# Optimization experiments

Measured on AMD Instinct MI355X. Metric: run time of the kernel, lower is better.

The kernel has to match this reference:

```python
import jax, jax.numpy as jnp
import numpy as np

# Fixed by JastrowNet source: ElectronicSchNet(n_interactions=2, kernel_dim=8, embedding_dim=16, version=1)
BATCH = 512
N_UP, N_DOWN = 16, 16
N_ELEC = N_UP + N_DOWN
N_ATOMS = 8
DIST_FEAT = 32
KERNEL = 8
EMBED = 16
N_LAYERS = 2
W_HIDDEN = 16  # log-spaced hidden dim of the w filter MLP: round(sqrt(32*8))
N_CHAN = 3     # same-spin, anti-spin, nuclear filter channels


def ssp(x):
    # shifted softplus used by SchNet
    return jax.nn.softplus(x) - jnp.log(2.0).astype(x.dtype)


def setup_inputs() -> dict:
    key = jax.random.key(0)
    ks = jax.random.split(key, 16)
    s = lambda fan_in: 1.0 / np.sqrt(fan_in)
    inp = {
        # Gaussian-expanded distance features are non-negative
        'edges_elec': jax.random.uniform(ks[0], (BATCH, N_ELEC, N_ELEC, DIST_FEAT), jnp.float32),
        'edges_nuc': jax.random.uniform(ks[1], (BATCH, N_ELEC, N_ATOMS, DIST_FEAT), jnp.float32),
        # electron spin embedding table (up=0, down=1) and nuclear embeddings Y
        'X_emb': jax.random.normal(ks[2], (2, EMBED), jnp.float32),
        'Y': jax.random.normal(ks[3], (N_ATOMS, KERNEL), jnp.float32),
        # per-layer, per-channel w filter MLP (dist_feat -> hidden -> kernel)
        'wW1': jax.random.normal(ks[4], (N_LAYERS, N_CHAN, DIST_FEAT, W_HIDDEN), jnp.float32) * s(DIST_FEAT),
        'wb1': jnp.zeros((N_LAYERS, N_CHAN, W_HIDDEN), jnp.float32),
        'wW2': jax.random.normal(ks[5], (N_LAYERS, N_CHAN, W_HIDDEN, KERNEL), jnp.float32) * s(W_HIDDEN),
        'wb2': jnp.zeros((N_LAYERS, N_CHAN, KERNEL), jnp.float32),
        # per-layer h subnet (embed -> kernel) and g subnet (kernel -> embed)
        'hW': jax.random.normal(ks[6], (N_LAYERS, EMBED, KERNEL), jnp.float32) * s(EMBED),
        'hb': jnp.zeros((N_LAYERS, KERNEL), jnp.float32),
        'gW': jax.random.normal(ks[7], (N_LAYERS, KERNEL, EMBED), jnp.float32) * s(KERNEL),
        'gb': jnp.zeros((N_LAYERS, EMBED), jnp.float32),
        # readout: Linear(16, 1, bias=False)
        'orb_W': jax.random.normal(ks[8], (EMBED,), jnp.float32) * s(EMBED),
    }
    return inp


def reference(edges_elec, edges_nuc, X_emb, Y, wW1, wb1, wW2, wb2, hW, hb, gW, gb, orb_W):
    B = edges_elec.shape[0]
    spins = jnp.concatenate([jnp.zeros(N_UP, jnp.int32), jnp.ones(N_DOWN, jnp.int32)])
    not_self = ~jnp.eye(N_ELEC, dtype=bool)
    same = ((spins[:, None] == spins[None, :]) & not_self)  # [n,n]
    anti = (spins[:, None] != spins[None, :])

    # initial electron embeddings by spin, broadcast over batch
    x = jnp.broadcast_to(X_emb[spins], (B, N_ELEC, EMBED))

    for l in range(N_LAYERS):
        def w_sub(e, c):
            h1 = ssp(e @ wW1[l, c] + wb1[l, c])
            return ssp(h1 @ wW2[l, c] + wb2[l, c])  # [..., KERNEL]

        w_same = w_sub(edges_elec, 0) * same[None, :, :, None]  # [B,n,n,k]
        w_anti = w_sub(edges_elec, 1) * anti[None, :, :, None]
        w_n = w_sub(edges_nuc, 2)                                # [B,n,m,k]

        hx = ssp(x @ hW[l] + hb[l])                              # [B,n,k]
        # continuous-filter message passing: gather neighbor features, multiply by filter, scatter-sum
        z = jnp.einsum('bijk,bjk->bik', w_same + w_anti, hx)
        z = z + jnp.einsum('bimk,mk->bik', w_n, Y)
        # version 1: single g applied to combined message, residual update
        x = x + z @ gW[l] + gb[l]

    # orbital readout Linear(16,1,bias=False).squeeze(-1).sum(-1)
    return (x @ orb_W).sum(axis=-1)  # [B]
```

## Files before the change

### kernel.cpp

```cpp
#include <hip/hip_runtime.h>
#include <hip/hip_bf16.h>
#include <cstddef>


#define NB   512
#define NE   32
#define NA   8
#define NF   32
#define NH   16
#define NK   8
#define NEMB 16

__device__ __forceinline__ float ssp(float v){
    return fmaxf(v, 0.f) + __logf(1.f + __expf(-fabsf(v))) - 0.6931471805599453f;
}

__device__ __forceinline__ void compute_w(const float4 ev[8],
        const float* __restrict__ sW1, const float* __restrict__ sB1,
        const float* __restrict__ sW2, const float* __restrict__ sB2,
        float w[NK])
{
    float h1[NH];
#pragma unroll
    for (int h = 0; h < NH; h++) h1[h] = sB1[h];
#pragma unroll
    for (int q = 0; q < 8; q++){
        float e4[4] = {ev[q].x, ev[q].y, ev[q].z, ev[q].w};
#pragma unroll
        for (int c = 0; c < 4; c++){
            const float ef = e4[c];
            const float4* w4 = (const float4*)(sW1 + (4*q + c)*NH);
#pragma unroll
            for (int t = 0; t < 4; t++){
                float4 wv = w4[t];
                h1[4*t+0] = fmaf(ef, wv.x, h1[4*t+0]);
                h1[4*t+1] = fmaf(ef, wv.y, h1[4*t+1]);
                h1[4*t+2] = fmaf(ef, wv.z, h1[4*t+2]);
                h1[4*t+3] = fmaf(ef, wv.w, h1[4*t+3]);
            }
        }
    }
#pragma unroll
    for (int h = 0; h < NH; h++) h1[h] = ssp(h1[h]);
    float acc[NK];
#pragma unroll
    for (int k = 0; k < NK; k++) acc[k] = sB2[k];
#pragma unroll
    for (int h = 0; h < NH; h++){
        const float hv = h1[h];
        const float4* w4 = (const float4*)(sW2 + h*NK);
#pragma unroll
        for (int t = 0; t < 2; t++){
            float4 wv = w4[t];
            acc[4*t+0] = fmaf(hv, wv.x, acc[4*t+0]);
            acc[4*t+1] = fmaf(hv, wv.y, acc[4*t+1]);
            acc[4*t+2] = fmaf(hv, wv.z, acc[4*t+2]);
            acc[4*t+3] = fmaf(hv, wv.w, acc[4*t+3]);
        }
    }
#pragma unroll
    for (int k = 0; k < NK; k++) w[k] = ssp(acc[k]);
}

extern "C" __global__ void __launch_bounds__(256, 4)
filters_kernel(const float* __restrict__ edges_elec,
               const float* __restrict__ edges_nuc,
               const float* __restrict__ X_emb,
               const float* __restrict__ Yk,
               const float* __restrict__ wW1, const float* __restrict__ wb1,
               const float* __restrict__ wW2, const float* __restrict__ wb2,
               const float* __restrict__ hW,  const float* __restrict__ hb,
               __hip_bfloat16* __restrict__ w2out,
               float* __restrict__ z1p,
               float* __restrict__ zn1, float* __restrict__ zn2)
{
    __shared__ __align__(16) float s_W1[2*NF*NH];
    __shared__ __align__(16) float s_b1[2*NH];
    __shared__ __align__(16) float s_W2[2*NH*NK];
    __shared__ __align__(16) float s_b2[2*NK];
    __shared__ float s_hx1[2*NK];
    __shared__ float s_Y[NA*NK];

    const int bid = blockIdx.x, t = threadIdx.x;
    const int p = bid >> 9, b = bid & 511;
    const bool isNuc = (p == 4);
    const int qi = p >> 1, qj = p & 1;
    const int cc = isNuc ? 2 : ((qi == qj) ? 0 : 1);

    for (int idx = t; idx < 2*NF*NH; idx += 256){
        int l = idx >> 9, r = idx & 511;
        s_W1[idx] = wW1[(l*3 + cc)*NF*NH + r];
    }
    if (t < 2*NH*NK){
        int l = t >> 7, r = t & 127;
        s_W2[t] = wW2[(l*3 + cc)*NH*NK + r];
    }
    if (t < 2*NH){ int l = t >> 4, r = t & 15; s_b1[t] = wb1[(l*3 + cc)*NH + r]; }
    if (t < 2*NK){ int l = t >> 3, r = t & 7;  s_b2[t] = wb2[(l*3 + cc)*NK + r]; }
    if (isNuc){
        if (t < NA*NK) s_Y[t] = Yk[t];
    } else if (t < 2*NK){
        int s = t >> 3, k = t & 7;
        float acc = hb[k];
#pragma unroll
        for (int e = 0; e < NEMB; e++)
            acc = fmaf(X_emb[s*NEMB + e], hW[e*NK + k], acc);
        s_hx1[t] = ssp(acc);
    }
    __syncthreads();

    const float* src;
    if (isNuc) src = edges_nuc + ((size_t)b*NE*NA + t) * NF;
    else {
        int i = qi*16 + (t >> 4), j = qj*16 + (t & 15);
        src = edges_elec + ((size_t)b*NE*NE + i*NE + j) * NF;
    }
    float4 ev[8];
    {
        const float4* p4 = (const float4*)src;
#pragma unroll
        for (int q = 0; q < 8; q++) ev[q] = p4[q];
    }

    {
        float w[NK];
        compute_w(ev, s_W1, s_b1, s_W2, s_b2, w);
        if (isNuc){
            const int m = t & 7, i = t >> 3;
            float pk[NK];
#pragma unroll
            for (int k = 0; k < NK; k++) pk[k] = w[k] * s_Y[m*NK + k];
#pragma unroll
            for (int off = 4; off > 0; off >>= 1)
#pragma unroll
                for (int k = 0; k < NK; k++) pk[k] += __shfl_down(pk[k], off, 8);
            if (m == 0){
#pragma unroll
                for (int k = 0; k < NK; k++) zn1[((size_t)b*NE + i)*NK + k] = pk[k];
            }
        } else {
            const int i16 = t >> 4, j16 = t & 15;
            const float msk = (cc == 0 && i16 == j16) ? 0.f : 1.f;
            float pk[NK];
#pragma unroll
            for (int k = 0; k < NK; k++) pk[k] = w[k] * msk * s_hx1[qj*NK + k];
#pragma unroll
            for (int off = 8; off > 0; off >>= 1)
#pragma unroll
                for (int k = 0; k < NK; k++) pk[k] += __shfl_down(pk[k], off, 16);
            if (j16 == 0){
                const int i = qi*16 + i16;
#pragma unroll
                for (int k = 0; k < NK; k++)
                    z1p[(((size_t)b*2 + qj)*NE + i)*NK + k] = pk[k];
            }
        }
    }
    {
        float w[NK];
        compute_w(ev, s_W1 + NF*NH, s_b1 + NH, s_W2 + NH*NK, s_b2 + NK, w);
        if (isNuc){
            const int m = t & 7, i = t >> 3;
            float pk[NK];
#pragma unroll
            for (int k = 0; k < NK; k++) pk[k] = w[k] * s_Y[m*NK + k];
#pragma unroll
            for (int off = 4; off > 0; off >>= 1)
#pragma unroll
                for (int k = 0; k < NK; k++) pk[k] += __shfl_down(pk[k], off, 8);
            if (m == 0){
#pragma unroll
                for (int k = 0; k < NK; k++) zn2[((size_t)b*NE + i)*NK + k] = pk[k];
            }
        } else {
            const int i16 = t >> 4, j16 = t & 15;
            const float msk = (cc == 0 && i16 == j16) ? 0.f : 1.f;
            const int i = qi*16 + i16, j = qj*16 + j16;
            union { __hip_bfloat16 h[8]; uint4 u; } pack;
#pragma unroll
            for (int k = 0; k < NK; k++) pack.h[k] = __float2bfloat16(w[k] * msk);
            *(uint4*)&w2out[((size_t)b*NE*NE + i*NE + j)*NK] = pack.u;
        }
    }
}

extern "C" __global__ void __launch_bounds__(256, 4)
update_kernel(const float* __restrict__ X_emb,
              const float* __restrict__ hW,  const float* __restrict__ hb,
              const float* __restrict__ gW,  const float* __restrict__ gb,
              const float* __restrict__ orbW,
              const __hip_bfloat16* __restrict__ w2,
              const float* __restrict__ z1p,
              const float* __restrict__ zn1, const float* __restrict__ zn2,
              float* __restrict__ out)
{
    __shared__ float s_x[NE*NEMB];
    __shared__ float s_z[NE*NK];
    __shared__ float s_hx[NE*NK];
    __shared__ float s_gW[2*NK*NEMB];
    __shared__ float s_gb[2*NEMB];
    __shared__ float s_hW1[NEMB*NK];
    __shared__ float s_hb1[NK];
    __shared__ float s_orb[NEMB];
    __shared__ float s_red[4];

    const int b = blockIdx.x, t = threadIdx.x;

    s_gW[t] = gW[t];
    if (t < 2*NEMB)  s_gb[t]  = gb[t];
    if (t < NEMB*NK) s_hW1[t] = hW[NEMB*NK + t];
    if (t < NK)      s_hb1[t] = hb[NK + t];
    if (t < NEMB)    s_orb[t] = orbW[t];
    {
        const int i = t >> 3, k = t & 7;
        s_z[t] = z1p[(((size_t)b*2 + 0)*NE + i)*NK + k]
               + z1p[(((size_t)b*2 + 1)*NE + i)*NK + k]
               + zn1[((size_t)b*NE + i)*NK + k];
    }
    __syncthreads();
#pragma unroll
    for (int q = 0; q < 2; q++){
        const int idx = q*256 + t, i = idx >> 4, e = idx & 15;
        float acc = s_gb[e];
#pragma unroll
        for (int k = 0; k < NK; k++)
            acc = fmaf(s_z[i*NK + k], s_gW[k*NEMB + e], acc);
        s_x[idx] = X_emb[(i >> 4)*NEMB + e] + acc;
    }
    __syncthreads();
    {
        const int i = t >> 3, k = t & 7;
        float acc = s_hb1[k];
#pragma unroll
        for (int e = 0; e < NEMB; e++)
            acc = fmaf(s_x[i*NEMB + e], s_hW1[e*NK + k], acc);
        s_hx[t] = ssp(acc);
    }
    __syncthreads();
    {
        const int i16 = t >> 4, j16 = t & 15;
#pragma unroll
        for (int qh = 0; qh < 2; qh++){
            const int i = qh*16 + i16;
            float zacc[NK];
#pragma unroll
            for (int k = 0; k < NK; k++) zacc[k] = 0.f;
#pragma unroll
            for (int qj = 0; qj < 2; qj++){
                const int j = qj*16 + j16;
                union { uint4 u; __hip_bfloat16 h[8]; } raw;
                raw.u = *(const uint4*)&w2[((size_t)b*NE*NE + i*NE + j)*NK];
                float pk[NK];
#pragma unroll
                for (int k = 0; k < NK; k++)
                    pk[k] = __bfloat162float(raw.h[k]) * s_hx[j*NK + k];
#pragma unroll
                for (int off = 8; off > 0; off >>= 1)
#pragma unroll
                    for (int k = 0; k < NK; k++) pk[k] += __shfl_down(pk[k], off, 16);
#pragma unroll
                for (int k = 0; k < NK; k++) zacc[k] += pk[k];
            }
            if (j16 == 0){
#pragma unroll
                for (int k = 0; k < NK; k++) s_z[i*NK + k] = zacc[k];
            }
        }
    }
    __syncthreads();
    { const int i = t >> 3, k = t & 7; s_z[t] += zn2[((size_t)b*NE + i)*NK + k]; }
    __syncthreads();
#pragma unroll
    for (int q = 0; q < 2; q++){
        const int idx = q*256 + t, i = idx >> 4, e = idx & 15;
        float acc = s_gb[NEMB + e];
#pragma unroll
        for (int k = 0; k < NK; k++)
            acc = fmaf(s_z[i*NK + k], s_gW[NK*NEMB + k*NEMB + e], acc);
        s_x[idx] += acc;
    }
    __syncthreads();
    float part = (s_x[t] + s_x[t + 256]) * s_orb[t & 15];
#pragma unroll
    for (int off = 32; off > 0; off >>= 1) part += __shfl_down(part, off, 64);
    if ((t & 63) == 0) s_red[t >> 6] = part;
    __syncthreads();
    if (t == 0) out[b] = s_red[0] + s_red[1] + s_red[2] + s_red[3];
}

extern "C" void kernel_launch(void* const* d_in, const int* in_sizes, int n_in,
                              void* d_out, int out_size, void* d_ws, size_t ws_size,
                              hipStream_t stream)
{
    const float* edges_elec = (const float*)d_in[0];
    const float* edges_nuc  = (const float*)d_in[1];
    const float* X_emb      = (const float*)d_in[2];
    const float* Yk         = (const float*)d_in[3];
    const float* wW1        = (const float*)d_in[4];
    const float* wb1        = (const float*)d_in[5];
    const float* wW2        = (const float*)d_in[6];
    const float* wb2        = (const float*)d_in[7];
    const float* hW         = (const float*)d_in[8];
    const float* hb         = (const float*)d_in[9];
    const float* gW         = (const float*)d_in[10];
    const float* gb         = (const float*)d_in[11];
    const float* orbW       = (const float*)d_in[12];

    char* ws = (char*)d_ws;
    __hip_bfloat16* w2 = (__hip_bfloat16*)ws;
    float* z1p = (float*)(ws + 8388608);
    float* zn1 = (float*)(ws + 8388608 + 1048576);
    float* zn2 = (float*)(ws + 8388608 + 1048576 + 524288);

    filters_kernel<<<5*NB, 256, 0, stream>>>(
        edges_elec, edges_nuc, X_emb, Yk, wW1, wb1, wW2, wb2, hW, hb,
        w2, z1p, zn1, zn2);
    update_kernel<<<NB, 256, 0, stream>>>(
        X_emb, hW, hb, gW, gb, orbW, w2, z1p, zn1, zn2, (float*)d_out);
}
```

Before: 157.8 us.

## Fuse filter and update kernels via per-batch atomic last-block completion

Merges the two launches into one kernel. Each of the five blocks per batch element increments a global counter, and the last block to finish runs the update and readout stage for that batch. Filter weights are now read straight from global memory (scalar loads) instead of being staged in LDS, and the layer-2 message sum is done per-thread over j instead of with shuffle reductions. This removes one launch and the inter-kernel gap, at the cost of a serial tail in the last block and relying on threadfence/atomic ordering.

```diff
diff --git a/kernel.cpp b/kernel.cpp
--- a/kernel.cpp
+++ b/kernel.cpp
@@ -11,75 +11,73 @@
 #define NK   8
 #define NEMB 16
 
+#define Z1P_OFF  8388608u
+#define ZN1_OFF  (Z1P_OFF + 1048576u)
+#define ZN2_OFF  (ZN1_OFF + 524288u)
+
+__device__ int g_cnt[NB];
+
 __device__ __forceinline__ float ssp(float v){
     return fmaxf(v, 0.f) + __logf(1.f + __expf(-fabsf(v))) - 0.6931471805599453f;
 }
 
 __device__ __forceinline__ void compute_w(const float4 ev[8],
-        const float* __restrict__ sW1, const float* __restrict__ sB1,
-        const float* __restrict__ sW2, const float* __restrict__ sB2,
+        const float* __restrict__ W1, const float* __restrict__ B1,
+        const float* __restrict__ W2, const float* __restrict__ B2,
         float w[NK])
 {
     float h1[NH];
 #pragma unroll
-    for (int h = 0; h < NH; h++) h1[h] = sB1[h];
+    for (int h = 0; h < NH; h++) h1[h] = B1[h];
 #pragma unroll
     for (int q = 0; q < 8; q++){
-        float e4[4] = {ev[q].x, ev[q].y, ev[q].z, ev[q].w};
+        const float e4[4] = {ev[q].x, ev[q].y, ev[q].z, ev[q].w};
 #pragma unroll
         for (int c = 0; c < 4; c++){
             const float ef = e4[c];
-            const float4* w4 = (const float4*)(sW1 + (4*q + c)*NH);
-#pragma unroll
-            for (int t = 0; t < 4; t++){
-                float4 wv = w4[t];
-                h1[4*t+0] = fmaf(ef, wv.x, h1[4*t+0]);
-                h1[4*t+1] = fmaf(ef, wv.y, h1[4*t+1]);
-                h1[4*t+2] = fmaf(ef, wv.z, h1[4*t+2]);
-                h1[4*t+3] = fmaf(ef, wv.w, h1[4*t+3]);
-            }
+            const float* wr = W1 + (4*q + c)*NH;
+#pragma unroll
+            for (int h = 0; h < NH; h++) h1[h] = fmaf(ef, wr[h], h1[h]);
         }
     }
 #pragma unroll
     for (int h = 0; h < NH; h++) h1[h] = ssp(h1[h]);
     float acc[NK];
 #pragma unroll
-    for (int k = 0; k < NK; k++) acc[k] = sB2[k];
+    for (int k = 0; k < NK; k++) acc[k] = B2[k];
 #pragma unroll
     for (int h = 0; h < NH; h++){
         const float hv = h1[h];
-        const float4* w4 = (const float4*)(sW2 + h*NK);
-#pragma unroll
-        for (int t = 0; t < 2; t++){
-            float4 wv = w4[t];
-            acc[4*t+0] = fmaf(hv, wv.x, acc[4*t+0]);
-            acc[4*t+1] = fmaf(hv, wv.y, acc[4*t+1]);
-            acc[4*t+2] = fmaf(hv, wv.z, acc[4*t+2]);
-            acc[4*t+3] = fmaf(hv, wv.w, acc[4*t+3]);
-        }
+        const float* wr = W2 + h*NK;
+#pragma unroll
+        for (int k = 0; k < NK; k++) acc[k] = fmaf(hv, wr[k], acc[k]);
     }
 #pragma unroll
     for (int k = 0; k < NK; k++) w[k] = ssp(acc[k]);
 }
 
 extern "C" __global__ void __launch_bounds__(256, 4)
-filters_kernel(const float* __restrict__ edges_elec,
-               const float* __restrict__ edges_nuc,
-               const float* __restrict__ X_emb,
-               const float* __restrict__ Yk,
-               const float* __restrict__ wW1, const float* __restrict__ wb1,
-               const float* __restrict__ wW2, const float* __restrict__ wb2,
-               const float* __restrict__ hW,  const float* __restrict__ hb,
-               __hip_bfloat16* __restrict__ w2out,
-               float* __restrict__ z1p,
-               float* __restrict__ zn1, float* __restrict__ zn2)
+jastrow_fused(const float* __restrict__ edges_elec,
+              const float* __restrict__ edges_nuc,
+              const float* __restrict__ X_emb,
+              const float* __restrict__ Yk,
+              const float* __restrict__ wW1, const float* __restrict__ wb1,
+              const float* __restrict__ wW2, const float* __restrict__ wb2,
+              const float* __restrict__ hW,  const float* __restrict__ hb,
+              const float* __restrict__ gW,  const float* __restrict__ gb,
+              const float* __restrict__ orbW,
+              __hip_bfloat16* __restrict__ w2,
+              float* __restrict__ z1p,
+              float* __restrict__ zn1, float* __restrict__ zn2,
+              float* __restrict__ out)
 {
-    __shared__ __align__(16) float s_W1[2*NF*NH];
-    __shared__ __align__(16) float s_b1[2*NH];
-    __shared__ __align__(16) float s_W2[2*NH*NK];
-    __shared__ __align__(16) float s_b2[2*NK];
-    __shared__ float s_hx1[2*NK];
+    __shared__ float s_hx1[NK];
     __shared__ float s_Y[NA*NK];
+    __shared__ float s_x[NE*NEMB];
+    __shared__ float s_z[NE*NK];
+    __shared__ float s_hx[NE*NK];
+    __shared__ float s_red[4];
+    __shared__ int   s_last;
 
     const int bid = blockIdx.x, t = threadIdx.x;
     const int p = bid >> 9, b = bid & 511;
@@ -87,24 +85,22 @@
     const int qi = p >> 1, qj = p & 1;
     const int cc = isNuc ? 2 : ((qi == qj) ? 0 : 1);
 
-    for (int idx = t; idx < 2*NF*NH; idx += 256){
-        int l = idx >> 9, r = idx & 511;
-        s_W1[idx] = wW1[(l*3 + cc)*NF*NH + r];
-    }
-    if (t < 2*NH*NK){
-        int l = t >> 7, r = t & 127;
-        s_W2[t] = wW2[(l*3 + cc)*NH*NK + r];
-    }
-    if (t < 2*NH){ int l = t >> 4, r = t & 15; s_b1[t] = wb1[(l*3 + cc)*NH + r]; }
-    if (t < 2*NK){ int l = t >> 3, r = t & 7;  s_b2[t] = wb2[(l*3 + cc)*NK + r]; }
+    const float* W1l0 = wW1 + (0*3 + cc)*NF*NH;
+    const float* W1l1 = wW1 + (1*3 + cc)*NF*NH;
+    const float* B1l0 = wb1 + (0*3 + cc)*NH;
+    const float* B1l1 = wb1 + (1*3 + cc)*NH;
+    const float* W2l0 = wW2 + (0*3 + cc)*NH*NK;
+    const float* W2l1 = wW2 + (1*3 + cc)*NH*NK;
+    const float* B2l0 = wb2 + (0*3 + cc)*NK;
+    const float* B2l1 = wb2 + (1*3 + cc)*NK;
+
     if (isNuc){
         if (t < NA*NK) s_Y[t] = Yk[t];
-    } else if (t < 2*NK){
-        int s = t >> 3, k = t & 7;
-        float acc = hb[k];
+    } else if (t < NK){
+        float acc = hb[t];
 #pragma unroll
         for (int e = 0; e < NEMB; e++)
-            acc = fmaf(X_emb[s*NEMB + e], hW[e*NK + k], acc);
+            acc = fmaf(X_emb[qj*NEMB + e], hW[e*NK + t], acc);
         s_hx1[t] = ssp(acc);
     }
     __syncthreads();
@@ -112,7 +108,7 @@
     const float* src;
     if (isNuc) src = edges_nuc + ((size_t)b*NE*NA + t) * NF;
     else {
-        int i = qi*16 + (t >> 4), j = qj*16 + (t & 15);
+        const int i = qi*16 + (t >> 4), j = qj*16 + (t & 15);
         src = edges_elec + ((size_t)b*NE*NE + i*NE + j) * NF;
     }
     float4 ev[8];
@@ -124,9 +120,9 @@
 
     {
         float w[NK];
-        compute_w(ev, s_W1, s_b1, s_W2, s_b2, w);
+        compute_w(ev, W1l0, B1l0, W2l0, B2l0, w);
         if (isNuc){
-            const int m = t & 7, i = t >> 3;
+            const int i = t >> 3, m = t & 7;
             float pk[NK];
 #pragma unroll
             for (int k = 0; k < NK; k++) pk[k] = w[k] * s_Y[m*NK + k];
@@ -143,7 +139,7 @@
             const float msk = (cc == 0 && i16 == j16) ? 0.f : 1.f;
             float pk[NK];
 #pragma unroll
-            for (int k = 0; k < NK; k++) pk[k] = w[k] * msk * s_hx1[qj*NK + k];
+            for (int k = 0; k < NK; k++) pk[k] = w[k] * msk * s_hx1[k];
 #pragma unroll
             for (int off = 8; off > 0; off >>= 1)
 #pragma unroll
@@ -158,9 +154,9 @@
     }
     {
         float w[NK];
-        compute_w(ev, s_W1 + NF*NH, s_b1 + NH, s_W2 + NH*NK, s_b2 + NK, w);
+        compute_w(ev, W1l1, B1l1, W2l1, B2l1, w);
         if (isNuc){
-            const int m = t & 7, i = t >> 3;
+            const int i = t >> 3, m = t & 7;
             float pk[NK];
 #pragma unroll
             for (int k = 0; k < NK; k++) pk[k] = w[k] * s_Y[m*NK + k];
@@ -179,108 +175,66 @@
             union { __hip_bfloat16 h[8]; uint4 u; } pack;
 #pragma unroll
             for (int k = 0; k < NK; k++) pack.h[k] = __float2bfloat16(w[k] * msk);
-            *(uint4*)&w2out[((size_t)b*NE*NE + i*NE + j)*NK] = pack.u;
+            *(uint4*)&w2[((size_t)b*NE*NE + i*NE + j)*NK] = pack.u;
         }
     }
-}
-
-extern "C" __global__ void __launch_bounds__(256, 4)
-update_kernel(const float* __restrict__ X_emb,
-              const float* __restrict__ hW,  const float* __restrict__ hb,
-              const float* __restrict__ gW,  const float* __restrict__ gb,
-              const float* __restrict__ orbW,
-              const __hip_bfloat16* __restrict__ w2,
-              const float* __restrict__ z1p,
-              const float* __restrict__ zn1, const float* __restrict__ zn2,
-              float* __restrict__ out)
-{
-    __shared__ float s_x[NE*NEMB];
-    __shared__ float s_z[NE*NK];
-    __shared__ float s_hx[NE*NK];
-    __shared__ float s_gW[2*NK*NEMB];
-    __shared__ float s_gb[2*NEMB];
-    __shared__ float s_hW1[NEMB*NK];
-    __shared__ float s_hb1[NK];
-    __shared__ float s_orb[NEMB];
-    __shared__ float s_red[4];
-
-    const int b = blockIdx.x, t = threadIdx.x;
-
-    s_gW[t] = gW[t];
-    if (t < 2*NEMB)  s_gb[t]  = gb[t];
-    if (t < NEMB*NK) s_hW1[t] = hW[NEMB*NK + t];
-    if (t < NK)      s_hb1[t] = hb[NK + t];
-    if (t < NEMB)    s_orb[t] = orbW[t];
-    {
-        const int i = t >> 3, k = t & 7;
-        s_z[t] = z1p[(((size_t)b*2 + 0)*NE + i)*NK + k]
-               + z1p[(((size_t)b*2 + 1)*NE + i)*NK + k]
-               + zn1[((size_t)b*NE + i)*NK + k];
-    }
+
+    __threadfence();
+    __syncthreads();
+    if (t == 0){
+        const int old = atomicAdd(&g_cnt[b], 1);
+        s_last = (old == 4) ? 1 : 0;
+        if (old == 4) atomicExch(&g_cnt[b], 0);
+    }
+    __syncthreads();
+    if (!s_last) return;
+    __threadfence();
+
+    s_z[t] = z1p[((size_t)b*2 + 0)*NE*NK + t]
+           + z1p[((size_t)b*2 + 1)*NE*NK + t]
+           + zn1[(size_t)b*NE*NK + t];
     __syncthreads();
 #pragma unroll
     for (int q = 0; q < 2; q++){
         const int idx = q*256 + t, i = idx >> 4, e = idx & 15;
-        float acc = s_gb[e];
+        float acc = gb[e];
 #pragma unroll
         for (int k = 0; k < NK; k++)
-            acc = fmaf(s_z[i*NK + k], s_gW[k*NEMB + e], acc);
+            acc = fmaf(s_z[i*NK + k], gW[k*NEMB + e], acc);
         s_x[idx] = X_emb[(i >> 4)*NEMB + e] + acc;
     }
     __syncthreads();
     {
         const int i = t >> 3, k = t & 7;
-        float acc = s_hb1[k];
+        float acc = hb[NK + k];
 #pragma unroll
         for (int e = 0; e < NEMB; e++)
-            acc = fmaf(s_x[i*NEMB + e], s_hW1[e*NK + k], acc);
+            acc = fmaf(s_x[i*NEMB + e], hW[NEMB*NK + e*NK + k], acc);
         s_hx[t] = ssp(acc);
     }
     __syncthreads();
     {
-        const int i16 = t >> 4, j16 = t & 15;
-#pragma unroll
-        for (int qh = 0; qh < 2; qh++){
-            const int i = qh*16 + i16;
-            float zacc[NK];
-#pragma unroll
-            for (int k = 0; k < NK; k++) zacc[k] = 0.f;
-#pragma unroll
-            for (int qj = 0; qj < 2; qj++){
-                const int j = qj*16 + j16;
-                union { uint4 u; __hip_bfloat16 h[8]; } raw;
-                raw.u = *(const uint4*)&w2[((size_t)b*NE*NE + i*NE + j)*NK];
-                float pk[NK];
-#pragma unroll
-                for (int k = 0; k < NK; k++)
-                    pk[k] = __bfloat162float(raw.h[k]) * s_hx[j*NK + k];
-#pragma unroll
-                for (int off = 8; off > 0; off >>= 1)
-#pragma unroll
-                    for (int k = 0; k < NK; k++) pk[k] += __shfl_down(pk[k], off, 16);
-#pragma unroll
-                for (int k = 0; k < NK; k++) zacc[k] += pk[k];
-            }
-            if (j16 == 0){
-#pragma unroll
-                for (int k = 0; k < NK; k++) s_z[i*NK + k] = zacc[k];
-            }
-        }
-    }
-    __syncthreads();
-    { const int i = t >> 3, k = t & 7; s_z[t] += zn2[((size_t)b*NE + i)*NK + k]; }
+        const int i = t >> 3, k = t & 7;
+        const __hip_bfloat16* wrow = w2 + ((size_t)b*NE*NE + i*NE)*NK + k;
+        float acc = zn2[(size_t)b*NE*NK + t];
+#pragma unroll
+        for (int j = 0; j < NE; j++)
+            acc = fmaf(__bfloat162float(wrow[j*NK]), s_hx[j*NK + k], acc);
+        __syncthreads();
+        s_z[t] = acc;
+    }
     __syncthreads();
 #pragma unroll
     for (int q = 0; q < 2; q++){
         const int idx = q*256 + t, i = idx >> 4, e = idx & 15;
-        float acc = s_gb[NEMB + e];
+        float acc = gb[NEMB + e];
 #pragma unroll
         for (int k = 0; k < NK; k++)
-            acc = fmaf(s_z[i*NK + k], s_gW[NK*NEMB + k*NEMB + e], acc);
+            acc = fmaf(s_z[i*NK + k], gW[NK*NEMB + k*NEMB + e], acc);
         s_x[idx] += acc;
     }
     __syncthreads();
-    float part = (s_x[t] + s_x[t + 256]) * s_orb[t & 15];
+    float part = (s_x[t] + s_x[t + 256]) * orbW[t & 15];
 #pragma unroll
     for (int off = 32; off > 0; off >>= 1) part += __shfl_down(part, off, 64);
     if ((t & 63) == 0) s_red[t >> 6] = part;
@@ -292,29 +246,17 @@
                               void* d_out, int out_size, void* d_ws, size_t ws_size,
                               hipStream_t stream)
 {
-    const float* edges_elec = (const float*)d_in[0];
-    const float* edges_nuc  = (const float*)d_in[1];
-    const float* X_emb      = (const float*)d_in[2];
-    const float* Yk         = (const float*)d_in[3];
-    const float* wW1        = (const float*)d_in[4];
-    const float* wb1        = (const float*)d_in[5];
-    const float* wW2        = (const float*)d_in[6];
-    const float* wb2        = (const float*)d_in[7];
-    const float* hW         = (const float*)d_in[8];
-    const float* hb         = (const float*)d_in[9];
-    const float* gW         = (const float*)d_in[10];
-    const float* gb         = (const float*)d_in[11];
-    const float* orbW       = (const float*)d_in[12];
-
     char* ws = (char*)d_ws;
     __hip_bfloat16* w2 = (__hip_bfloat16*)ws;
-    float* z1p = (float*)(ws + 8388608);
-    float* zn1 = (float*)(ws + 8388608 + 1048576);
-    float* zn2 = (float*)(ws + 8388608 + 1048576 + 524288);
-
-    filters_kernel<<<5*NB, 256, 0, stream>>>(
-        edges_elec, edges_nuc, X_emb, Yk, wW1, wb1, wW2, wb2, hW, hb,
-        w2, z1p, zn1, zn2);
-    update_kernel<<<NB, 256, 0, stream>>>(
-        X_emb, hW, hb, gW, gb, orbW, w2, z1p, zn1, zn2, (float*)d_out);
-}
+    float* z1p = (float*)(ws + Z1P_OFF);
+    float* zn1 = (float*)(ws + ZN1_OFF);
+    float* zn2 = (float*)(ws + ZN2_OFF);
+
+    jastrow_fused<<<5*NB, 256, 0, stream>>>(
+        (const float*)d_in[0],  (const float*)d_in[1],  (const float*)d_in[2],
+        (const float*)d_in[3],  (const float*)d_in[4],  (const float*)d_in[5],
+        (const float*)d_in[6],  (const float*)d_in[7],  (const float*)d_in[8],
+        (const float*)d_in[9],  (const float*)d_in[10], (const float*)d_in[11],
+        (const float*)d_in[12],
+        w2, z1p, zn1, zn2, (float*)d_out);
+}
```

After: 367.4 us. 2.33x slower.

## Regroup filter blocks by layer and channel, evaluate two edges per thread with packed FMA

Applied to the files above, without the earlier changes.

Filter blocks are re-partitioned so each block handles a single layer and channel (same-spin or anti-spin, or nuclear over two batches). Each thread now evaluates the MLP on two edges using v2f packed FMAs that share weight loads, and shared memory holds only one layer's weights. Edge rows are read from global memory once per layer instead of once for both layers, so edge traffic doubles, but per-block weight staging shrinks and the launch bound rises to 6 blocks. The packed math is meant to lower ALU and LDS instruction counts.

```diff
diff --git a/kernel.cpp b/kernel.cpp
--- a/kernel.cpp
+++ b/kernel.cpp
@@ -11,58 +11,86 @@
 #define NK   8
 #define NEMB 16
 
+#define Z1P_OFF  8388608u
+#define ZN1_OFF  (Z1P_OFF + 1048576u)
+#define ZN2_OFF  (ZN1_OFF + 524288u)
+
+typedef float v2f __attribute__((ext_vector_type(2)));
+
 __device__ __forceinline__ float ssp(float v){
     return fmaxf(v, 0.f) + __logf(1.f + __expf(-fabsf(v))) - 0.6931471805599453f;
 }
 
-__device__ __forceinline__ void compute_w(const float4 ev[8],
-        const float* __restrict__ sW1, const float* __restrict__ sB1,
-        const float* __restrict__ sW2, const float* __restrict__ sB2,
-        float w[NK])
+__device__ __forceinline__ void mlp2(const float* __restrict__ rA,
+                                     const float* __restrict__ rB,
+                                     const float* __restrict__ sW1,
+                                     const float* __restrict__ sb1,
+                                     const float* __restrict__ sW2,
+                                     const float* __restrict__ sb2,
+                                     float wout[2][NK])
 {
-    float h1[NH];
-#pragma unroll
-    for (int h = 0; h < NH; h++) h1[h] = sB1[h];
+    v2f h[2][8];
+    const v2f* b1 = (const v2f*)sb1;
+#pragma unroll
+    for (int u = 0; u < 8; u++){ h[0][u] = b1[u]; h[1][u] = b1[u]; }
+
 #pragma unroll
     for (int q = 0; q < 8; q++){
-        float e4[4] = {ev[q].x, ev[q].y, ev[q].z, ev[q].w};
-#pragma unroll
-        for (int c = 0; c < 4; c++){
-            const float ef = e4[c];
-            const float4* w4 = (const float4*)(sW1 + (4*q + c)*NH);
-#pragma unroll
-            for (int t = 0; t < 4; t++){
-                float4 wv = w4[t];
-                h1[4*t+0] = fmaf(ef, wv.x, h1[4*t+0]);
-                h1[4*t+1] = fmaf(ef, wv.y, h1[4*t+1]);
-                h1[4*t+2] = fmaf(ef, wv.z, h1[4*t+2]);
-                h1[4*t+3] = fmaf(ef, wv.w, h1[4*t+3]);
-            }
-        }
-    }
-#pragma unroll
-    for (int h = 0; h < NH; h++) h1[h] = ssp(h1[h]);
-    float acc[NK];
-#pragma unroll
-    for (int k = 0; k < NK; k++) acc[k] = sB2[k];
-#pragma unroll
-    for (int h = 0; h < NH; h++){
-        const float hv = h1[h];
-        const float4* w4 = (const float4*)(sW2 + h*NK);
-#pragma unroll
-        for (int t = 0; t < 2; t++){
-            float4 wv = w4[t];
-            acc[4*t+0] = fmaf(hv, wv.x, acc[4*t+0]);
-            acc[4*t+1] = fmaf(hv, wv.y, acc[4*t+1]);
-            acc[4*t+2] = fmaf(hv, wv.z, acc[4*t+2]);
-            acc[4*t+3] = fmaf(hv, wv.w, acc[4*t+3]);
-        }
-    }
-#pragma unroll
-    for (int k = 0; k < NK; k++) w[k] = ssp(acc[k]);
-}
-
-extern "C" __global__ void __launch_bounds__(256, 4)
+        const float4 fA = ((const float4*)rA)[q];
+        const float4 fB = ((const float4*)rB)[q];
+#pragma unroll
+        for (int c4 = 0; c4 < 4; c4++){
+            const v2f* wr = (const v2f*)(sW1 + (q*4 + c4)*NH);
+            const float eA = (c4==0)?fA.x:(c4==1)?fA.y:(c4==2)?fA.z:fA.w;
+            const float eB = (c4==0)?fB.x:(c4==1)?fB.y:(c4==2)?fB.z:fB.w;
+            const v2f vA = {eA, eA}, vB = {eB, eB};
+#pragma unroll
+            for (int u = 0; u < 8; u++){
+                const v2f wv = wr[u];
+                h[0][u] = __builtin_elementwise_fma(vA, wv, h[0][u]);
+                h[1][u] = __builtin_elementwise_fma(vB, wv, h[1][u]);
+            }
+        }
+    }
+#pragma unroll
+    for (int s = 0; s < 2; s++)
+#pragma unroll
+        for (int u = 0; u < 8; u++){
+            h[s][u].x = ssp(h[s][u].x);
+            h[s][u].y = ssp(h[s][u].y);
+        }
+
+    v2f a[2][4];
+    const v2f* b2 = (const v2f*)sb2;
+#pragma unroll
+    for (int u = 0; u < 4; u++){ a[0][u] = b2[u]; a[1][u] = b2[u]; }
+#pragma unroll
+    for (int u = 0; u < 8; u++){
+#pragma unroll
+        for (int half = 0; half < 2; half++){
+            const int hh = 2*u + half;
+            const v2f* wr = (const v2f*)(sW2 + hh*NK);
+            const float hA = half ? h[0][u].y : h[0][u].x;
+            const float hB = half ? h[1][u].y : h[1][u].x;
+            const v2f vA = {hA, hA}, vB = {hB, hB};
+#pragma unroll
+            for (int u2 = 0; u2 < 4; u2++){
+                const v2f wv = wr[u2];
+                a[0][u2] = __builtin_elementwise_fma(vA, wv, a[0][u2]);
+                a[1][u2] = __builtin_elementwise_fma(vB, wv, a[1][u2]);
+            }
+        }
+    }
+#pragma unroll
+    for (int s = 0; s < 2; s++)
+#pragma unroll
+        for (int u = 0; u < 4; u++){
+            wout[s][2*u]   = ssp(a[s][u].x);
+            wout[s][2*u+1] = ssp(a[s][u].y);
+        }
+}
+
+extern "C" __global__ void __launch_bounds__(256, 6)
 filters_kernel(const float* __restrict__ edges_elec,
                const float* __restrict__ edges_nuc,
                const float* __restrict__ X_emb,
@@ -74,112 +102,105 @@
                float* __restrict__ z1p,
                float* __restrict__ zn1, float* __restrict__ zn2)
 {
-    __shared__ __align__(16) float s_W1[2*NF*NH];
-    __shared__ __align__(16) float s_b1[2*NH];
-    __shared__ __align__(16) float s_W2[2*NH*NK];
-    __shared__ __align__(16) float s_b2[2*NK];
+    __shared__ __align__(16) float s_W1[NF*NH];
+    __shared__ __align__(16) float s_b1[NH];
+    __shared__ __align__(16) float s_W2[NH*NK];
+    __shared__ __align__(16) float s_b2[NK];
     __shared__ float s_hx1[2*NK];
     __shared__ float s_Y[NA*NK];
 
     const int bid = blockIdx.x, t = threadIdx.x;
-    const int p = bid >> 9, b = bid & 511;
-    const bool isNuc = (p == 4);
-    const int qi = p >> 1, qj = p & 1;
-    const int cc = isNuc ? 2 : ((qi == qj) ? 0 : 1);
-
-    for (int idx = t; idx < 2*NF*NH; idx += 256){
-        int l = idx >> 9, r = idx & 511;
-        s_W1[idx] = wW1[(l*3 + cc)*NF*NH + r];
-    }
-    if (t < 2*NH*NK){
-        int l = t >> 7, r = t & 127;
-        s_W2[t] = wW2[(l*3 + cc)*NH*NK + r];
-    }
-    if (t < 2*NH){ int l = t >> 4, r = t & 15; s_b1[t] = wb1[(l*3 + cc)*NH + r]; }
-    if (t < 2*NK){ int l = t >> 3, r = t & 7;  s_b2[t] = wb2[(l*3 + cc)*NK + r]; }
+    const bool isNuc = (bid >= 4*NB);
+    int b, c, l, bA;
+    if (isNuc){
+        const int idx = bid - 4*NB;
+        l = idx & 1; bA = 2*(idx >> 1); b = bA; c = 0;
+    } else {
+        b = bid >> 2; c = (bid >> 1) & 1; l = bid & 1; bA = b;
+    }
+    const int cc = isNuc ? 2 : c;
+
+    for (int i2 = t; i2 < NF*NH; i2 += 256) s_W1[i2] = wW1[(l*3 + cc)*NF*NH + i2];
+    if (t < NH*NK) s_W2[t] = wW2[(l*3 + cc)*NH*NK + t];
+    if (t < NH)    s_b1[t] = wb1[(l*3 + cc)*NH + t];
+    if (t < NK)    s_b2[t] = wb2[(l*3 + cc)*NK + t];
     if (isNuc){
         if (t < NA*NK) s_Y[t] = Yk[t];
-    } else if (t < 2*NK){
-        int s = t >> 3, k = t & 7;
+    } else if (l == 0 && t < 2*NK){
+        const int sp = t >> 3, k = t & 7;
         float acc = hb[k];
 #pragma unroll
         for (int e = 0; e < NEMB; e++)
-            acc = fmaf(X_emb[s*NEMB + e], hW[e*NK + k], acc);
+            acc = fmaf(X_emb[sp*NEMB + e], hW[e*NK + k], acc);
         s_hx1[t] = ssp(acc);
     }
     __syncthreads();
 
-    const float* src;
-    if (isNuc) src = edges_nuc + ((size_t)b*NE*NA + t) * NF;
-    else {
-        int i = qi*16 + (t >> 4), j = qj*16 + (t & 15);
-        src = edges_elec + ((size_t)b*NE*NE + i*NE + j) * NF;
-    }
-    float4 ev[8];
-    {
-        const float4* p4 = (const float4*)src;
-#pragma unroll
-        for (int q = 0; q < 8; q++) ev[q] = p4[q];
-    }
-
-    {
-        float w[NK];
-        compute_w(ev, s_W1, s_b1, s_W2, s_b2, w);
-        if (isNuc){
-            const int m = t & 7, i = t >> 3;
+    const int i16 = t >> 4, j16 = t & 15;
+    const float* rA;
+    const float* rB;
+    if (isNuc){
+        rA = edges_nuc + ((size_t)(bA + 0)*NE*NA + t) * NF;
+        rB = edges_nuc + ((size_t)(bA + 1)*NE*NA + t) * NF;
+    } else {
+        const int qj0 = c ? 1 : 0, qj1 = c ? 0 : 1;
+        rA = edges_elec + (((size_t)b*NE +      i16)*NE + qj0*16 + j16) * NF;
+        rB = edges_elec + (((size_t)b*NE + 16 + i16)*NE + qj1*16 + j16) * NF;
+    }
+
+    float w[2][NK];
+    mlp2(rA, rB, s_W1, s_b1, s_W2, s_b2, w);
+
+    if (isNuc){
+        const int i = t >> 3, m = t & 7;
+        float* zn = (l == 0) ? zn1 : zn2;
+#pragma unroll
+        for (int s = 0; s < 2; s++){
             float pk[NK];
 #pragma unroll
-            for (int k = 0; k < NK; k++) pk[k] = w[k] * s_Y[m*NK + k];
+            for (int k = 0; k < NK; k++) pk[k] = w[s][k] * s_Y[m*NK + k];
 #pragma unroll
             for (int off = 4; off > 0; off >>= 1)
 #pragma unroll
                 for (int k = 0; k < NK; k++) pk[k] += __shfl_down(pk[k], off, 8);
             if (m == 0){
 #pragma unroll
-                for (int k = 0; k < NK; k++) zn1[((size_t)b*NE + i)*NK + k] = pk[k];
+                for (int k = 0; k < NK; k++)
+                    zn[((size_t)(bA + s)*NE + i)*NK + k] = pk[k];
+            }
+        }
+    } else {
+        const float msk = (c == 0 && i16 == j16) ? 0.f : 1.f;
+        if (l == 0){
+#pragma unroll
+            for (int s = 0; s < 2; s++){
+                const int qj = c ? (1 - s) : s;
+                float pk[NK];
+#pragma unroll
+                for (int k = 0; k < NK; k++)
+                    pk[k] = w[s][k] * msk * s_hx1[qj*NK + k];
+#pragma unroll
+                for (int off = 8; off > 0; off >>= 1)
+#pragma unroll
+                    for (int k = 0; k < NK; k++) pk[k] += __shfl_down(pk[k], off, 16);
+                if (j16 == 0){
+                    const int i = s*16 + i16;
+#pragma unroll
+                    for (int k = 0; k < NK; k++)
+                        z1p[(((size_t)b*2 + c)*NE + i)*NK + k] = pk[k];
+                }
             }
         } else {
-            const int i16 = t >> 4, j16 = t & 15;
-            const float msk = (cc == 0 && i16 == j16) ? 0.f : 1.f;
-            float pk[NK];
-#pragma unroll
-            for (int k = 0; k < NK; k++) pk[k] = w[k] * msk * s_hx1[qj*NK + k];
-#pragma unroll
-            for (int off = 8; off > 0; off >>= 1)
-#pragma unroll
-                for (int k = 0; k < NK; k++) pk[k] += __shfl_down(pk[k], off, 16);
-            if (j16 == 0){
-                const int i = qi*16 + i16;
+#pragma unroll
+            for (int s = 0; s < 2; s++){
+                const int qj = c ? (1 - s) : s;
+                const int i = s*16 + i16, j = qj*16 + j16;
+                union { __hip_bfloat16 h[8]; uint4 u; } pack;
 #pragma unroll
                 for (int k = 0; k < NK; k++)
-                    z1p[(((size_t)b*2 + qj)*NE + i)*NK + k] = pk[k];
-            }
-        }
-    }
-    {
-        float w[NK];
-        compute_w(ev, s_W1 + NF*NH, s_b1 + NH, s_W2 + NH*NK, s_b2 + NK, w);
-        if (isNuc){
-            const int m = t & 7, i = t >> 3;
-            float pk[NK];
-#pragma unroll
-            for (int k = 0; k < NK; k++) pk[k] = w[k] * s_Y[m*NK + k];
-#pragma unroll
-            for (int off = 4; off > 0; off >>= 1)
-#pragma unroll
-                for (int k = 0; k < NK; k++) pk[k] += __shfl_down(pk[k], off, 8);
-            if (m == 0){
-#pragma unroll
-                for (int k = 0; k < NK; k++) zn2[((size_t)b*NE + i)*NK + k] = pk[k];
-            }
-        } else {
-            const int i16 = t >> 4, j16 = t & 15;
-            const float msk = (cc == 0 && i16 == j16) ? 0.f : 1.f;
-            const int i = qi*16 + i16, j = qj*16 + j16;
-            union { __hip_bfloat16 h[8]; uint4 u; } pack;
-#pragma unroll
-            for (int k = 0; k < NK; k++) pack.h[k] = __float2bfloat16(w[k] * msk);
-            *(uint4*)&w2out[((size_t)b*NE*NE + i*NE + j)*NK] = pack.u;
+                    pack.h[k] = __float2bfloat16(w[s][k] * msk);
+                *(uint4*)&w2out[((size_t)b*NE*NE + i*NE + j)*NK] = pack.u;
+            }
         }
     }
 }
@@ -308,11 +329,11 @@
 
     char* ws = (char*)d_ws;
     __hip_bfloat16* w2 = (__hip_bfloat16*)ws;
-    float* z1p = (float*)(ws + 8388608);
-    float* zn1 = (float*)(ws + 8388608 + 1048576);
-    float* zn2 = (float*)(ws + 8388608 + 1048576 + 524288);
-
-    filters_kernel<<<5*NB, 256, 0, stream>>>(
+    float* z1p = (float*)(ws + Z1P_OFF);
+    float* zn1 = (float*)(ws + ZN1_OFF);
+    float* zn2 = (float*)(ws + ZN2_OFF);
+
+    filters_kernel<<<4*NB + NB, 256, 0, stream>>>(
         edges_elec, edges_nuc, X_emb, Yk, wW1, wb1, wW2, wb2, hW, hb,
         w2, z1p, zn1, zn2);
     update_kernel<<<NB, 256, 0, stream>>>(
```

Result: slower. 211.1 us (+33.7%).
